# Optimization experiments

Measured on AMD Instinct MI355X. Metric: run time of the kernel, lower is better.

## Reference

```python
import jax, jax.numpy as jnp
import numpy as np

N = 100000       # nodes
E = 3200000      # edges (avg degree 32)
NFEAT = 128
NHID = 128
NCLASS = 64


def setup_inputs() -> dict:
    key = jax.random.key(0)
    ks = jax.random.split(key, 8)
    x = jax.random.normal(ks[0], (N, NFEAT), dtype=jnp.float32)
    edge_index = jax.random.randint(ks[1], (2, E), 0, N, dtype=jnp.int64)
    s1 = 1.0 / np.sqrt(NFEAT)
    s2 = 1.0 / np.sqrt(NHID)
    return {
        "x": x,
        "edge_index": edge_index,
        "W1_self": jax.random.normal(ks[2], (NFEAT, NHID), dtype=jnp.float32) * s1,
        "W1_neigh": jax.random.normal(ks[3], (NFEAT, NHID), dtype=jnp.float32) * s1,
        "b1": jnp.zeros((NHID,), dtype=jnp.float32),
        "W2_self": jax.random.normal(ks[4], (NHID, NCLASS), dtype=jnp.float32) * s2,
        "W2_neigh": jax.random.normal(ks[5], (NHID, NCLASS), dtype=jnp.float32) * s2,
        "b2": jnp.zeros((NCLASS,), dtype=jnp.float32),
    }


def _sage_conv(h, src, dst, inv_deg, W_self, W_neigh, b):
    # gather source features, scatter-add to destinations, mean-normalize
    agg = jax.ops.segment_sum(h[src], dst, num_segments=N)  # [N, F]
    mean = agg * inv_deg[:, None]
    return h @ W_self + mean @ W_neigh + b


def reference(x, edge_index, W1_self, W1_neigh, b1, W2_self, W2_neigh, b2):
    src, dst = edge_index[0], edge_index[1]
    deg = jax.ops.segment_sum(jnp.ones((E,), dtype=x.dtype), dst, num_segments=N)
    inv_deg = 1.0 / jnp.maximum(deg, 1.0)
    h = _sage_conv(x, src, dst, inv_deg, W1_self, W1_neigh, b1)
    h = jax.nn.relu(h)
    # F.dropout with training=False is identity (inference mode)
    out = _sage_conv(h, src, dst, inv_deg, W2_self, W2_neigh, b2)
    return out
```

## Files before the change

### kernel.cpp

```cpp
#include <hip/hip_runtime.h>

#define NNODES 100000
#define NEDGES 3200000
#define NBKT 196
#define NTILES2 1563
#define NGB 1563

typedef unsigned int uint;
typedef unsigned short ushort;
typedef unsigned char uchar;
typedef __attribute__((ext_vector_type(8))) short short8;
typedef __attribute__((ext_vector_type(4))) float f32x4;
typedef __attribute__((ext_vector_type(2))) float f32x2;

__device__ inline ushort bf16_rne(float f) {
    uint u = __float_as_uint(f);
    return (ushort)((u + 0x7FFFu + ((u >> 16) & 1u)) >> 16);
}
__device__ inline uint pack_bf2(float a, float b) {
    return (uint)bf16_rne(a) | ((uint)bf16_rne(b) << 16);
}
__device__ inline float2 unpack_bf2(uint v) {
    float2 r;
    r.x = __uint_as_float(v << 16);
    r.y = __uint_as_float(v & 0xFFFF0000u);
    return r;
}

__device__ inline uchar f32_to_fp8(float f) {
    uint u = __float_as_uint(f);
    uint s = (u >> 24) & 0x80u;
    uint e = (u >> 23) & 0xFFu;
    if (e < 121u) return (uchar)s;
    uint m = u & 0x7FFFFFu;
    uint r = (m + 0x7FFFFu + ((m >> 20) & 1u)) >> 20;
    uint em = ((e - 120u) << 3) + r;
    return (uchar)(s | em);
}
__device__ inline float fp8_dec(uint b) {
    uint s = (b & 0x80u) << 24;
    uint em = b & 0x7Fu;
    float v = __uint_as_float(s | ((em + 960u) << 20));
    return em ? v : 0.0f;
}
__device__ inline float2 fp8_lo2(uint pk) {
#if __has_builtin(__builtin_amdgcn_cvt_pk_f32_fp8)
    f32x2 r = __builtin_amdgcn_cvt_pk_f32_fp8((int)pk, false);
    return make_float2(r[0], r[1]);
#else
    return make_float2(fp8_dec(pk & 0xFFu), fp8_dec((pk >> 8) & 0xFFu));
#endif
}
__device__ inline float2 fp8_hi2(uint pk) {
#if __has_builtin(__builtin_amdgcn_cvt_pk_f32_fp8)
    f32x2 r = __builtin_amdgcn_cvt_pk_f32_fp8((int)pk, true);
    return make_float2(r[0], r[1]);
#else
    return make_float2(fp8_dec((pk >> 16) & 0xFFu), fp8_dec(pk >> 24));
#endif
}

__global__ __launch_bounds__(256) void histprep_kernel(
    const int* __restrict__ dst, int* __restrict__ bhist,
    const float* __restrict__ W1s, const float* __restrict__ W1n,
    const float* __restrict__ W2s, const float* __restrict__ W2n,
    ushort* __restrict__ wt) {
    if (blockIdx.x >= 128) {
        const int id = (blockIdx.x - 128) * 256 + threadIdx.x;
        const int m = id >> 14;
        const int r = id & 16383;
        const int c = r >> 7;
        const int k = r & 127;
        float v;
        if (m == 0) v = W1s[k * 128 + c];
        else if (m == 1) v = W1n[k * 128 + c];
        else v = (c < 64) ? W2s[k * 64 + c] : W2n[k * 64 + (c - 64)];
        wt[id] = bf16_rne(v);
        return;
    }
    __shared__ int lh[NBKT];
    for (int i = threadIdx.x; i < NBKT; i += 256) lh[i] = 0;
    __syncthreads();
    const int n4 = NEDGES / 4;
    for (int i = blockIdx.x * 256 + threadIdx.x; i < n4; i += 128 * 256) {
        const int4 d = ((const int4*)dst)[i];
        atomicAdd(&lh[d.x >> 9], 1);
        atomicAdd(&lh[d.y >> 9], 1);
        atomicAdd(&lh[d.z >> 9], 1);
        atomicAdd(&lh[d.w >> 9], 1);
    }
    __syncthreads();
    for (int i = threadIdx.x; i < NBKT; i += 256)
        if (lh[i]) atomicAdd(&bhist[i], lh[i]);
}

__global__ __launch_bounds__(256) void scan_bkt(const int* __restrict__ bhist,
                                                int* __restrict__ boff,
                                                int* __restrict__ gcur,
                                                int* __restrict__ rs) {
    __shared__ int s[256];
    const int tid = threadIdx.x;
    const int v = (tid < NBKT) ? bhist[tid] : 0;
    s[tid] = v;
    __syncthreads();
    for (int ofs = 1; ofs < 256; ofs <<= 1) {
        int t = (tid >= ofs) ? s[tid - ofs] : 0;
        __syncthreads();
        s[tid] += t;
        __syncthreads();
    }
    const int excl = s[tid] - v;
    if (tid < NBKT) {
        boff[tid] = excl;
        gcur[tid] = excl;
    }
    if (tid == NBKT - 1) {
        boff[NBKT] = s[tid];
        rs[NNODES] = NEDGES;
    }
}

__global__ __launch_bounds__(256) void megaA_kernel(
    const float* __restrict__ x, const ushort* __restrict__ wt,
    const float* __restrict__ b1, ushort* __restrict__ hbf,
    uchar* __restrict__ xnf8, const int* __restrict__ src,
    const int* __restrict__ dst, int* __restrict__ gcur,
    uint* __restrict__ pairbuf) {
    __shared__ uint4 sWq[2048];
    const int bid = blockIdx.x;
    const int tid = threadIdx.x;

    if (bid & 1) {
        int* lhist = (int*)sWq;
        int* gbl = (int*)sWq + 256;
        const int t = bid >> 1;
        const int ebase = t * 2048;
        const int n = min(2048, NEDGES - ebase);
        const int nv4 = n >> 2;
        lhist[tid] = 0;
        __syncthreads();
        int4 sv[2], dv[2];
        int rk[2][4];
#pragma unroll
        for (int u = 0; u < 2; ++u) {
            const int i4 = tid + 256 * u;
            if (i4 < nv4) {
                sv[u] = ((const int4*)(src + ebase))[i4];
                dv[u] = ((const int4*)(dst + ebase))[i4];
                rk[u][0] = atomicAdd(&lhist[dv[u].x >> 9], 1);
                rk[u][1] = atomicAdd(&lhist[dv[u].y >> 9], 1);
                rk[u][2] = atomicAdd(&lhist[dv[u].z >> 9], 1);
                rk[u][3] = atomicAdd(&lhist[dv[u].w >> 9], 1);
            }
        }
        __syncthreads();
        const int cnt = lhist[tid];
        if (tid < NBKT && cnt > 0) gbl[tid] = atomicAdd(&gcur[tid], cnt);
        __syncthreads();
#pragma unroll
        for (int u = 0; u < 2; ++u) {
            const int i4 = tid + 256 * u;
            if (i4 < nv4) {
                const int ss[4] = {sv[u].x, sv[u].y, sv[u].z, sv[u].w};
                const int dd[4] = {dv[u].x, dv[u].y, dv[u].z, dv[u].w};
#pragma unroll
                for (int j = 0; j < 4; ++j) {
                    const int b = dd[j] >> 9;
                    pairbuf[gbl[b] + rk[u][j]] =
                        ((uint)ss[j] << 9) | ((uint)dd[j] & 511u);
                }
            }
        }
        return;
    }

    const int g = bid >> 1;
    const int w = tid >> 6;
    const int l = tid & 63;
    const int lg = l >> 4;
    const int lr = l & 15;
    const int rowbase = g * 64;
    const int arow = min(rowbase + w * 16 + lr, NNODES - 1);
    const float* xrow = x + (size_t)arow * 128;
    short8 ahi[4], alo[4];
#pragma unroll
    for (int ks = 0; ks < 4; ++ks) {
        const float4 va = *(const float4*)&xrow[ks * 32 + lg * 8];
        const float4 vb = *(const float4*)&xrow[ks * 32 + lg * 8 + 4];
        const float vv[8] = {va.x, va.y, va.z, va.w, vb.x, vb.y, vb.z, vb.w};
        short8 h8, l8;
#pragma unroll
        for (int j = 0; j < 8; ++j) {
            const ushort hu = bf16_rne(vv[j]);
            h8[j] = (short)hu;
            l8[j] = (short)bf16_rne(vv[j] - __uint_as_float((uint)hu << 16));
        }
        ahi[ks] = h8;
        alo[ks] = l8;
    }

#pragma unroll
    for (int wsel = 0; wsel < 2; ++wsel) {
        __syncthreads();
#pragma unroll
        for (int i = 0; i < 8; ++i) {
            const int cid = tid + 256 * i;
            const int kc = cid & 15;
            const int c = cid >> 4;
            sWq[c * 16 + (kc ^ (c & 15))] =
                *(const uint4*)&wt[(size_t)(wsel * 2048 + cid) * 8];
        }
        __syncthreads();
#pragma unroll 4
        for (int ct = 0; ct < 8; ++ct) {
            f32x4 acc;
            if (wsel == 0) {
                const float bv = b1[ct * 16 + lr];
                acc = (f32x4){bv, bv, bv, bv};
            } else {
                acc = (f32x4){0.0f, 0.0f, 0.0f, 0.0f};
            }
            const int cbase = (ct * 16 + lr) * 16;
#pragma unroll
            for (int ks = 0; ks < 4; ++ks) {
                const short8 bf = *(const short8*)&sWq[cbase + ((4 * ks + lg) ^ lr)];
                acc = __builtin_amdgcn_mfma_f32_16x16x32_bf16(ahi[ks], bf, acc, 0, 0, 0);
                acc = __builtin_amdgcn_mfma_f32_16x16x32_bf16(alo[ks], bf, acc, 0, 0, 0);
            }
#pragma unroll
            for (int r_ = 0; r_ < 4; ++r_) {
                const int orow = rowbase + w * 16 + lg * 4 + r_;
                if (orow < NNODES) {
                    if (wsel == 0)
                        hbf[(size_t)orow * 128 + ct * 16 + lr] = bf16_rne(acc[r_]);
                    else
                        xnf8[(size_t)orow * 128 + ct * 16 + lr] = f32_to_fp8(acc[r_]);
                }
            }
        }
    }
}

__global__ __launch_bounds__(256) void bucket_kernel(const uint* __restrict__ pairbuf,
                                                     const int* __restrict__ boff,
                                                     int* __restrict__ rs,
                                                     float* __restrict__ invd,
                                                     int* __restrict__ ebuf) {
    __shared__ int ndeg[512];
    __shared__ int nofs[512];
    __shared__ int lcur[512];
    __shared__ int sps[256];
    const int b = blockIdx.x;
    const int tid = threadIdx.x;
    const int nb = b << 9;
    const int ln = min(512, NNODES - nb);
    const int base = boff[b];
    const int cnt = boff[b + 1] - base;
    for (int i = tid; i < 512; i += 256) {
        ndeg[i] = 0;
        lcur[i] = 0;
    }
    __syncthreads();
    for (int i = tid; i < cnt; i += 256) {
        atomicAdd(&ndeg[pairbuf[base + i] & 511u], 1);
    }
    __syncthreads();
    for (int nidx = tid; nidx < ln; nidx += 256)
        invd[nb + nidx] = 1.0f / fmaxf((float)ndeg[nidx], 1.0f);
    const int a0 = ndeg[2 * tid];
    const int a1 = ndeg[2 * tid + 1];
    sps[tid] = a0 + a1;
    __syncthreads();
    for (int ofs = 1; ofs < 256; ofs <<= 1) {
        int t = (tid >= ofs) ? sps[tid - ofs] : 0;
        __syncthreads();
        sps[tid] += t;
        __syncthreads();
    }
    const int excl = sps[tid] - (a0 + a1);
    nofs[2 * tid] = excl;
    nofs[2 * tid + 1] = excl + a0;
    __syncthreads();
    for (int nidx = tid; nidx < ln; nidx += 256) rs[nb + nidx] = base + nofs[nidx];
    for (int i = tid; i < cnt; i += 256) {
        const uint e = pairbuf[base + i];
        const int nn = (int)(e & 511u);
        const int p = atomicAdd(&lcur[nn], 1);
        ebuf[base + nofs[nn] + p] = (int)(e >> 9);
    }
}

__global__ __launch_bounds__(256) void gemm2_dual_kernel(
    const ushort* __restrict__ hbf, const ushort* __restrict__ wt2,
    const float* __restrict__ b2, float* __restrict__ out,
    uchar* __restrict__ hnf8) {
    __shared__ uint4 sWq[2048];
    const int tid = threadIdx.x;
#pragma unroll
    for (int i = 0; i < 8; ++i) {
        const int cid = tid + 256 * i;
        const int kc = cid & 15;
        const int c = cid >> 4;
        sWq[c * 16 + (kc ^ (c & 15))] = *(const uint4*)&wt2[cid * 8];
    }
    const int w = tid >> 6;
    const int l = tid & 63;
    const int lg = l >> 4;
    const int lr = l & 15;
    const int rowbase = blockIdx.x * 64;
    const int arow = min(rowbase + w * 16 + lr, NNODES - 1);
    const ushort* hrow = hbf + (size_t)arow * 128;
    short8 a[4];
#pragma unroll
    for (int ks = 0; ks < 4; ++ks) a[ks] = *(const short8*)&hrow[ks * 32 + lg * 8];
    __syncthreads();

#pragma unroll 4
    for (int ct = 0; ct < 8; ++ct) {
        f32x4 acc;
        if (ct < 4) {
            const float bv = b2[ct * 16 + lr];
            acc = (f32x4){bv, bv, bv, bv};
        } else {
            acc = (f32x4){0.0f, 0.0f, 0.0f, 0.0f};
        }
        const int cbase = (ct * 16 + lr) * 16;
#pragma unroll
        for (int ks = 0; ks < 4; ++ks) {
            const short8 bf = *(const short8*)&sWq[cbase + ((4 * ks + lg) ^ lr)];
            acc = __builtin_amdgcn_mfma_f32_16x16x32_bf16(a[ks], bf, acc, 0, 0, 0);
        }
#pragma unroll
        for (int r_ = 0; r_ < 4; ++r_) {
            const int orow = rowbase + w * 16 + lg * 4 + r_;
            if (orow < NNODES) {
                if (ct < 4)
                    out[(size_t)orow * 64 + ct * 16 + lr] = acc[r_];
                else
                    hnf8[(size_t)orow * 64 + (ct - 4) * 16 + lr] = f32_to_fp8(acc[r_]);
            }
        }
    }
}

__global__ __launch_bounds__(256) void agg1_kernel(const int* __restrict__ rs,
                                                   const int* __restrict__ ebuf,
                                                   const float* __restrict__ invd,
                                                   const uchar* __restrict__ xnf8,
                                                   ushort* __restrict__ hbf) {
    const int node = blockIdx.x * 8 + (threadIdx.x >> 5);
    if (node >= NNODES) return;
    const int lane = threadIdx.x & 31;
    const int beg = rs[node];
    const int end = rs[node + 1];
    const uint* fp = (const uint*)xnf8 + lane;
    float a0 = 0.0f, a1 = 0.0f, a2 = 0.0f, a3 = 0.0f;
    int i = beg;
    for (; i + 3 < end; i += 4) {
#pragma unroll
        for (int u = 0; u < 4; ++u) {
            const uint pk = fp[(size_t)ebuf[i + u] * 32];
            const float2 lo = fp8_lo2(pk);
            const float2 hi = fp8_hi2(pk);
            a0 += lo.x; a1 += lo.y; a2 += hi.x; a3 += hi.y;
        }
    }
    for (; i < end; ++i) {
        const uint pk = fp[(size_t)ebuf[i] * 32];
        const float2 lo = fp8_lo2(pk);
        const float2 hi = fp8_hi2(pk);
        a0 += lo.x; a1 += lo.y; a2 += hi.x; a3 += hi.y;
    }
    const float w = invd[node];
    uint* hp = (uint*)hbf + (size_t)node * 64 + lane * 2;
    uint2 hv = *(uint2*)hp;
    float2 h0 = unpack_bf2(hv.x);
    float2 h1 = unpack_bf2(hv.y);
    h0.x = fmaxf(fmaf(w, a0, h0.x), 0.0f);
    h0.y = fmaxf(fmaf(w, a1, h0.y), 0.0f);
    h1.x = fmaxf(fmaf(w, a2, h1.x), 0.0f);
    h1.y = fmaxf(fmaf(w, a3, h1.y), 0.0f);
    hv.x = pack_bf2(h0.x, h0.y);
    hv.y = pack_bf2(h1.x, h1.y);
    *(uint2*)hp = hv;
}

__global__ __launch_bounds__(256) void agg2_kernel(const int* __restrict__ rs,
                                                   const int* __restrict__ ebuf,
                                                   const float* __restrict__ invd,
                                                   const uchar* __restrict__ hnf8,
                                                   float* __restrict__ out) {
    const int node = blockIdx.x * 8 + (threadIdx.x >> 5);
    if (node >= NNODES) return;
    const int lane = threadIdx.x & 31;
    const int beg = rs[node];
    const int end = rs[node + 1];
    const ushort* fp = (const ushort*)hnf8 + lane;
    float a0 = 0.0f, a1 = 0.0f;
    int i = beg;
    for (; i + 3 < end; i += 4) {
#pragma unroll
        for (int u = 0; u < 4; ++u) {
            const uint pk = (uint)fp[(size_t)ebuf[i + u] * 32];
            const float2 v = fp8_lo2(pk);
            a0 += v.x; a1 += v.y;
        }
    }
    for (; i < end; ++i) {
        const uint pk = (uint)fp[(size_t)ebuf[i] * 32];
        const float2 v = fp8_lo2(pk);
        a0 += v.x; a1 += v.y;
    }
    const float w = invd[node];
    float2* op = (float2*)&out[(size_t)node * 64 + lane * 2];
    float2 ov = *op;
    ov.x = fmaf(w, a0, ov.x);
    ov.y = fmaf(w, a1, ov.y);
    *op = ov;
}

extern "C" void kernel_launch(void* const* d_in, const int* in_sizes, int n_in,
                              void* d_out, int out_size, void* d_ws, size_t ws_size,
                              hipStream_t stream) {
    const float* x   = (const float*)d_in[0];
    const int*   ei  = (const int*)d_in[1];
    const float* W1s = (const float*)d_in[2];
    const float* W1n = (const float*)d_in[3];
    const float* b1  = (const float*)d_in[4];
    const float* W2s = (const float*)d_in[5];
    const float* W2n = (const float*)d_in[6];
    const float* b2  = (const float*)d_in[7];
    float* out = (float*)d_out;

    const int* src = ei;
    const int* dst = ei + NEDGES;

    int* w = (int*)d_ws;
    int*    bhist   = w;
    int*    boff    = w + 256;
    int*    gcur    = w + 512;
    int*    rs      = w + 768;
    float*  invd    = (float*)(w + 100864);
    int*    ebuf    = w + 200864;
    uint*   pairbuf = (uint*)(w + 3400864);
    uchar*  xnf8    = (uchar*)(w + 6600864);
    ushort* hbf     = (ushort*)(w + 9800864);
    ushort* wtbuf   = (ushort*)(w + 16200864);
    uchar*  hnf8    = xnf8;

    hipMemsetAsync(bhist, 0, 256 * sizeof(int), stream);
    histprep_kernel<<<320, 256, 0, stream>>>(dst, bhist, W1s, W1n, W2s, W2n, wtbuf);
    scan_bkt<<<1, 256, 0, stream>>>(bhist, boff, gcur, rs);

    megaA_kernel<<<2 * NTILES2, 256, 0, stream>>>(x, wtbuf, b1, hbf, xnf8, src, dst,
                                                  gcur, pairbuf);
    bucket_kernel<<<NBKT, 256, 0, stream>>>(pairbuf, boff, rs, invd, ebuf);

    agg1_kernel<<<NNODES / 8, 256, 0, stream>>>(rs, ebuf, invd, xnf8, hbf);

    gemm2_dual_kernel<<<NGB, 256, 0, stream>>>(hbf, wtbuf + 32768, b2, out, hnf8);
    agg2_kernel<<<NNODES / 8, 256, 0, stream>>>(rs, ebuf, invd, hnf8, out);
}
```

Before: 264.3 us.

## Drop histogram pass with fixed-stride buckets and slice fp8 features for aggregation

Removes the dst histogram and bucket scan kernels by giving each destination bucket a fixed-capacity region (BSTRIDE) and per-node start and end arrays, so CSR construction no longer needs a pre-pass over the edges. Neighbour features in fp8 are stored as 32-column slices so each aggregation pass gathers 32-byte rows. Each aggregation kernel now runs several passes over the slices, with 8 edges processed in parallel per node and combined by wave shuffles. This lowers edge-read cost and improves gather locality, but ebuf must be read several times and correctness depends on no bucket exceeding its fixed capacity.

Result: slower. 411.1 us (+55.5%).

```diff
diff --git a/kernel.cpp b/kernel.cpp
--- a/kernel.cpp
+++ b/kernel.cpp
@@ -5,6 +5,9 @@
 #define NBKT 196
 #define NTILES2 1563
 #define NGB 1563
+#define BSTRIDE 18432
+#define EBUFSZ (NBKT * BSTRIDE)
+#define SLICEW 3200000
 
 typedef unsigned int uint;
 typedef unsigned short ushort;
@@ -60,64 +63,26 @@
 #endif
 }
 
-__global__ __launch_bounds__(256) void histprep_kernel(
-    const int* __restrict__ dst, int* __restrict__ bhist,
-    const float* __restrict__ W1s, const float* __restrict__ W1n,
-    const float* __restrict__ W2s, const float* __restrict__ W2n,
-    ushort* __restrict__ wt) {
-    if (blockIdx.x >= 128) {
-        const int id = (blockIdx.x - 128) * 256 + threadIdx.x;
-        const int m = id >> 14;
-        const int r = id & 16383;
-        const int c = r >> 7;
-        const int k = r & 127;
-        float v;
-        if (m == 0) v = W1s[k * 128 + c];
-        else if (m == 1) v = W1n[k * 128 + c];
-        else v = (c < 64) ? W2s[k * 64 + c] : W2n[k * 64 + (c - 64)];
-        wt[id] = bf16_rne(v);
+__global__ __launch_bounds__(256) void prep_kernel(const float* __restrict__ W1s,
+                                                   const float* __restrict__ W1n,
+                                                   const float* __restrict__ W2s,
+                                                   const float* __restrict__ W2n,
+                                                   ushort* __restrict__ wt,
+                                                   int* __restrict__ gcur) {
+    if (blockIdx.x == 192) {
+        gcur[threadIdx.x] = (int)threadIdx.x * BSTRIDE;
         return;
     }
-    __shared__ int lh[NBKT];
-    for (int i = threadIdx.x; i < NBKT; i += 256) lh[i] = 0;
-    __syncthreads();
-    const int n4 = NEDGES / 4;
-    for (int i = blockIdx.x * 256 + threadIdx.x; i < n4; i += 128 * 256) {
-        const int4 d = ((const int4*)dst)[i];
-        atomicAdd(&lh[d.x >> 9], 1);
-        atomicAdd(&lh[d.y >> 9], 1);
-        atomicAdd(&lh[d.z >> 9], 1);
-        atomicAdd(&lh[d.w >> 9], 1);
-    }
-    __syncthreads();
-    for (int i = threadIdx.x; i < NBKT; i += 256)
-        if (lh[i]) atomicAdd(&bhist[i], lh[i]);
-}
-
-__global__ __launch_bounds__(256) void scan_bkt(const int* __restrict__ bhist,
-                                                int* __restrict__ boff,
-                                                int* __restrict__ gcur,
-                                                int* __restrict__ rs) {
-    __shared__ int s[256];
-    const int tid = threadIdx.x;
-    const int v = (tid < NBKT) ? bhist[tid] : 0;
-    s[tid] = v;
-    __syncthreads();
-    for (int ofs = 1; ofs < 256; ofs <<= 1) {
-        int t = (tid >= ofs) ? s[tid - ofs] : 0;
-        __syncthreads();
-        s[tid] += t;
-        __syncthreads();
-    }
-    const int excl = s[tid] - v;
-    if (tid < NBKT) {
-        boff[tid] = excl;
-        gcur[tid] = excl;
-    }
-    if (tid == NBKT - 1) {
-        boff[NBKT] = s[tid];
-        rs[NNODES] = NEDGES;
-    }
+    const int id = blockIdx.x * 256 + threadIdx.x;
+    const int m = id >> 14;
+    const int r = id & 16383;
+    const int c = r >> 7;
+    const int k = r & 127;
+    float v;
+    if (m == 0) v = W1s[k * 128 + c];
+    else if (m == 1) v = W1n[k * 128 + c];
+    else v = (c < 64) ? W2s[k * 64 + c] : W2n[k * 64 + (c - 64)];
+    wt[id] = bf16_rne(v);
 }
 
 __global__ __launch_bounds__(256) void megaA_kernel(
@@ -231,10 +196,12 @@
             for (int r_ = 0; r_ < 4; ++r_) {
                 const int orow = rowbase + w * 16 + lg * 4 + r_;
                 if (orow < NNODES) {
-                    if (wsel == 0)
+                    if (wsel == 0) {
                         hbf[(size_t)orow * 128 + ct * 16 + lr] = bf16_rne(acc[r_]);
-                    else
-                        xnf8[(size_t)orow * 128 + ct * 16 + lr] = f32_to_fp8(acc[r_]);
+                    } else {
+                        xnf8[(size_t)(ct >> 1) * SLICEW + (size_t)orow * 32 +
+                             (ct & 1) * 16 + lr] = f32_to_fp8(acc[r_]);
+                    }
                 }
             }
         }
@@ -242,8 +209,9 @@
 }
 
 __global__ __launch_bounds__(256) void bucket_kernel(const uint* __restrict__ pairbuf,
-                                                     const int* __restrict__ boff,
+                                                     const int* __restrict__ gcur,
                                                      int* __restrict__ rs,
+                                                     int* __restrict__ re,
                                                      float* __restrict__ invd,
                                                      int* __restrict__ ebuf) {
     __shared__ int ndeg[512];
@@ -254,8 +222,8 @@
     const int tid = threadIdx.x;
     const int nb = b << 9;
     const int ln = min(512, NNODES - nb);
-    const int base = boff[b];
-    const int cnt = boff[b + 1] - base;
+    const int base = b * BSTRIDE;
+    const int cnt = gcur[b] - base;
     for (int i = tid; i < 512; i += 256) {
         ndeg[i] = 0;
         lcur[i] = 0;
@@ -281,7 +249,10 @@
     nofs[2 * tid] = excl;
     nofs[2 * tid + 1] = excl + a0;
     __syncthreads();
-    for (int nidx = tid; nidx < ln; nidx += 256) rs[nb + nidx] = base + nofs[nidx];
+    for (int nidx = tid; nidx < ln; nidx += 256) {
+        rs[nb + nidx] = base + nofs[nidx];
+        re[nb + nidx] = base + nofs[nidx] + ndeg[nidx];
+    }
     for (int i = tid; i < cnt; i += 256) {
         const uint e = pairbuf[base + i];
         const int nn = (int)(e & 511u);
@@ -334,89 +305,100 @@
         for (int r_ = 0; r_ < 4; ++r_) {
             const int orow = rowbase + w * 16 + lg * 4 + r_;
             if (orow < NNODES) {
-                if (ct < 4)
+                if (ct < 4) {
                     out[(size_t)orow * 64 + ct * 16 + lr] = acc[r_];
-                else
-                    hnf8[(size_t)orow * 64 + (ct - 4) * 16 + lr] = f32_to_fp8(acc[r_]);
+                } else {
+                    const int col2 = (ct - 4) * 16 + lr;
+                    hnf8[(size_t)(col2 >> 5) * SLICEW + (size_t)orow * 32 +
+                         (col2 & 31)] = f32_to_fp8(acc[r_]);
+                }
             }
         }
     }
 }
 
 __global__ __launch_bounds__(256) void agg1_kernel(const int* __restrict__ rs,
+                                                   const int* __restrict__ re,
                                                    const int* __restrict__ ebuf,
                                                    const float* __restrict__ invd,
                                                    const uchar* __restrict__ xnf8,
                                                    ushort* __restrict__ hbf) {
-    const int node = blockIdx.x * 8 + (threadIdx.x >> 5);
-    if (node >= NNODES) return;
-    const int lane = threadIdx.x & 31;
+    const int pass = blockIdx.x / 25000;
+    const int node = (blockIdx.x % 25000) * 4 + (threadIdx.x >> 6);
+    const int l = threadIdx.x & 63;
+    const int e = l >> 3;
+    const int c = l & 7;
     const int beg = rs[node];
-    const int end = rs[node + 1];
-    const uint* fp = (const uint*)xnf8 + lane;
+    const int end = re[node];
+    const uint* fp = (const uint*)(xnf8 + (size_t)pass * SLICEW) + c;
     float a0 = 0.0f, a1 = 0.0f, a2 = 0.0f, a3 = 0.0f;
-    int i = beg;
-    for (; i + 3 < end; i += 4) {
-#pragma unroll
-        for (int u = 0; u < 4; ++u) {
-            const uint pk = fp[(size_t)ebuf[i + u] * 32];
-            const float2 lo = fp8_lo2(pk);
-            const float2 hi = fp8_hi2(pk);
-            a0 += lo.x; a1 += lo.y; a2 += hi.x; a3 += hi.y;
-        }
-    }
-    for (; i < end; ++i) {
-        const uint pk = fp[(size_t)ebuf[i] * 32];
+    for (int i = beg + e; i < end; i += 8) {
+        const uint pk = fp[(size_t)ebuf[i] * 8];
         const float2 lo = fp8_lo2(pk);
         const float2 hi = fp8_hi2(pk);
         a0 += lo.x; a1 += lo.y; a2 += hi.x; a3 += hi.y;
     }
-    const float w = invd[node];
-    uint* hp = (uint*)hbf + (size_t)node * 64 + lane * 2;
-    uint2 hv = *(uint2*)hp;
-    float2 h0 = unpack_bf2(hv.x);
-    float2 h1 = unpack_bf2(hv.y);
-    h0.x = fmaxf(fmaf(w, a0, h0.x), 0.0f);
-    h0.y = fmaxf(fmaf(w, a1, h0.y), 0.0f);
-    h1.x = fmaxf(fmaf(w, a2, h1.x), 0.0f);
-    h1.y = fmaxf(fmaf(w, a3, h1.y), 0.0f);
-    hv.x = pack_bf2(h0.x, h0.y);
-    hv.y = pack_bf2(h1.x, h1.y);
-    *(uint2*)hp = hv;
+#pragma unroll
+    for (int m = 8; m < 64; m <<= 1) {
+        a0 += __shfl_xor(a0, m);
+        a1 += __shfl_xor(a1, m);
+        a2 += __shfl_xor(a2, m);
+        a3 += __shfl_xor(a3, m);
+    }
+    if (e == 0) {
+        const float w = invd[node];
+        uint* hp = (uint*)hbf + (size_t)node * 64 + pass * 16 + c * 2;
+        uint2 hv = *(uint2*)hp;
+        float2 h0 = unpack_bf2(hv.x);
+        float2 h1 = unpack_bf2(hv.y);
+        h0.x = fmaxf(fmaf(w, a0, h0.x), 0.0f);
+        h0.y = fmaxf(fmaf(w, a1, h0.y), 0.0f);
+        h1.x = fmaxf(fmaf(w, a2, h1.x), 0.0f);
+        h1.y = fmaxf(fmaf(w, a3, h1.y), 0.0f);
+        hv.x = pack_bf2(h0.x, h0.y);
+        hv.y = pack_bf2(h1.x, h1.y);
+        *(uint2*)hp = hv;
+    }
 }
 
 __global__ __launch_bounds__(256) void agg2_kernel(const int* __restrict__ rs,
+                                                   const int* __restrict__ re,
                                                    const int* __restrict__ ebuf,
                                                    const float* __restrict__ invd,
                                                    const uchar* __restrict__ hnf8,
                                                    float* __restrict__ out) {
-    const int node = blockIdx.x * 8 + (threadIdx.x >> 5);
-    if (node >= NNODES) return;
-    const int lane = threadIdx.x & 31;
+    const int pass = blockIdx.x / 25000;
+    const int node = (blockIdx.x % 25000) * 4 + (threadIdx.x >> 6);
+    const int l = threadIdx.x & 63;
+    const int e = l >> 3;
+    const int c = l & 7;
     const int beg = rs[node];
-    const int end = rs[node + 1];
-    const ushort* fp = (const ushort*)hnf8 + lane;
-    float a0 = 0.0f, a1 = 0.0f;
-    int i = beg;
-    for (; i + 3 < end; i += 4) {
-#pragma unroll
-        for (int u = 0; u < 4; ++u) {
-            const uint pk = (uint)fp[(size_t)ebuf[i + u] * 32];
-            const float2 v = fp8_lo2(pk);
-            a0 += v.x; a1 += v.y;
-        }
-    }
-    for (; i < end; ++i) {
-        const uint pk = (uint)fp[(size_t)ebuf[i] * 32];
-        const float2 v = fp8_lo2(pk);
-        a0 += v.x; a1 += v.y;
-    }
-    const float w = invd[node];
-    float2* op = (float2*)&out[(size_t)node * 64 + lane * 2];
-    float2 ov = *op;
-    ov.x = fmaf(w, a0, ov.x);
-    ov.y = fmaf(w, a1, ov.y);
-    *op = ov;
+    const int end = re[node];
+    const uint* fp = (const uint*)(hnf8 + (size_t)pass * SLICEW) + c;
+    float a0 = 0.0f, a1 = 0.0f, a2 = 0.0f, a3 = 0.0f;
+    for (int i = beg + e; i < end; i += 8) {
+        const uint pk = fp[(size_t)ebuf[i] * 8];
+        const float2 lo = fp8_lo2(pk);
+        const float2 hi = fp8_hi2(pk);
+        a0 += lo.x; a1 += lo.y; a2 += hi.x; a3 += hi.y;
+    }
+#pragma unroll
+    for (int m = 8; m < 64; m <<= 1) {
+        a0 += __shfl_xor(a0, m);
+        a1 += __shfl_xor(a1, m);
+        a2 += __shfl_xor(a2, m);
+        a3 += __shfl_xor(a3, m);
+    }
+    if (e == 0) {
+        const float w = invd[node];
+        float4* op = (float4*)&out[(size_t)node * 64 + pass * 32 + c * 4];
+        float4 ov = *op;
+        ov.x = fmaf(w, a0, ov.x);
+        ov.y = fmaf(w, a1, ov.y);
+        ov.z = fmaf(w, a2, ov.z);
+        ov.w = fmaf(w, a3, ov.w);
+        *op = ov;
+    }
 }
 
 extern "C" void kernel_launch(void* const* d_in, const int* in_sizes, int n_in,
@@ -436,28 +418,25 @@
     const int* dst = ei + NEDGES;
 
     int* w = (int*)d_ws;
-    int*    bhist   = w;
-    int*    boff    = w + 256;
-    int*    gcur    = w + 512;
-    int*    rs      = w + 768;
-    float*  invd    = (float*)(w + 100864);
-    int*    ebuf    = w + 200864;
-    uint*   pairbuf = (uint*)(w + 3400864);
-    uchar*  xnf8    = (uchar*)(w + 6600864);
-    ushort* hbf     = (ushort*)(w + 9800864);
-    ushort* wtbuf   = (ushort*)(w + 16200864);
+    int*    gcur    = w;
+    int*    rs      = w + 256;
+    int*    re      = w + 100256;
+    float*  invd    = (float*)(w + 200256);
+    int*    ebuf    = w + 300256;
+    uint*   pairbuf = (uint*)(w + 3912928);
+    uchar*  xnf8    = (uchar*)(w + 7525600);
+    ushort* hbf     = (ushort*)(w + 10725600);
+    ushort* wtbuf   = (ushort*)(w + 17125600);
     uchar*  hnf8    = xnf8;
 
-    hipMemsetAsync(bhist, 0, 256 * sizeof(int), stream);
-    histprep_kernel<<<320, 256, 0, stream>>>(dst, bhist, W1s, W1n, W2s, W2n, wtbuf);
-    scan_bkt<<<1, 256, 0, stream>>>(bhist, boff, gcur, rs);
+    prep_kernel<<<193, 256, 0, stream>>>(W1s, W1n, W2s, W2n, wtbuf, gcur);
 
     megaA_kernel<<<2 * NTILES2, 256, 0, stream>>>(x, wtbuf, b1, hbf, xnf8, src, dst,
                                                   gcur, pairbuf);
-    bucket_kernel<<<NBKT, 256, 0, stream>>>(pairbuf, boff, rs, invd, ebuf);
-
-    agg1_kernel<<<NNODES / 8, 256, 0, stream>>>(rs, ebuf, invd, xnf8, hbf);
+    bucket_kernel<<<NBKT, 256, 0, stream>>>(pairbuf, gcur, rs, re, invd, ebuf);
+
+    agg1_kernel<<<100000, 256, 0, stream>>>(rs, re, ebuf, invd, xnf8, hbf);
 
     gemm2_dual_kernel<<<NGB, 256, 0, stream>>>(hbf, wtbuf + 32768, b2, out, hnf8);
-    agg2_kernel<<<NNODES / 8, 256, 0, stream>>>(rs, ebuf, invd, hnf8, out);
-}
+    agg2_kernel<<<50000, 256, 0, stream>>>(rs, re, ebuf, invd, hnf8, out);
+}
```
